# Optimization experiments

Measured on AMD Instinct MI355X. Metric: run time of the kernel, lower is better.

Reference implementation:

```python
import jax, jax.numpy as jnp
import numpy as np

B, CIN, COUT, K, L = 16, 512, 512, 3, 8192
STRIDE, PAD, DIL = 1, 1, 1  # 'same' conv: Lout == L


def setup_inputs() -> dict:
    key = jax.random.key(0)
    k1, k2, k3 = jax.random.split(key, 3)
    x = jax.random.normal(k1, (B, CIN, L), dtype=jnp.float32)
    # int8 quantized weight stored as int32 for portability; values in [-128, 127]
    qweight = jax.random.randint(k2, (COUT, CIN, K), -128, 128, dtype=jnp.int32)
    scale = jnp.float32(0.01)  # per-tensor dequant scale (w_max / 127)
    bias = jax.random.normal(k3, (COUT,), dtype=jnp.float32)
    return {"x": x, "qweight": qweight, "scale": scale, "bias": bias}


def reference(x, qweight, scale, bias):
    # Dequantize: fp32 weight = int8 * scale (materialized every call, as in torch module)
    w = (qweight.astype(jnp.float32) * scale).astype(x.dtype)
    out = jax.lax.conv_general_dilated(
        x, w,
        window_strides=(STRIDE,),
        padding=[(PAD, PAD)],
        rhs_dilation=(DIL,),
        dimension_numbers=("NCH", "OIH", "NCH"),
        feature_group_count=1,
    )
    return out + bias.astype(x.dtype)[None, :, None]
```

## Files before the change

kernel.cpp:

```cpp
#include <hip/hip_runtime.h>
#include <hip/hip_bf16.h>

#define CIN   512
#define COUT  512
#define LEN   8192
#define NB    16
#define KW    3
#define PROWS 8200

#define WB_ELEMS (COUT * CIN * KW)
#define WB_BYTES ((size_t)WB_ELEMS * 2)
#define XS_BYTES ((size_t)NB * PROWS * CIN * 2)

#define BM2 256
#define BN2 256
#define BK3 64
#define NT  ((CIN / BK3) * KW)
#define TILE3 (BM2 * BK3 * 2)

typedef __attribute__((ext_vector_type(4))) float f32x4;
typedef __attribute__((ext_vector_type(8))) short bf16x8;

static __device__ __forceinline__ unsigned short f2bf(float f) {
    union { float f; unsigned u; } cv; cv.f = f;
    return (unsigned short)((cv.u + 0x7fffu + ((cv.u >> 16) & 1u)) >> 16);
}

__global__ __launch_bounds__(256) void wconv_kernel(const int* __restrict__ q,
                                                    unsigned short* __restrict__ wb) {
    int idx = blockIdx.x * 256 + threadIdx.x;
    if (idx >= WB_ELEMS) return;
    int co = idx / (KW * CIN);
    int r  = idx - co * (KW * CIN);
    int t  = r >> 9;
    int ci = r & 511;
    wb[idx] = f2bf((float)q[(co * CIN + ci) * KW + t]);
}

__global__ __launch_bounds__(256) void xprep_kernel(const float* __restrict__ x,
                                                    unsigned short* __restrict__ xs) {
    __shared__ char T[64 * 132];
    int blk = blockIdx.x;
    int b   = blk >> 10;
    int ci0 = ((blk >> 7) & 7) * 64;
    int l0  = (blk & 127) * 64;
    int tid = threadIdx.x;

    if (l0 == 0 && tid < 64)
        xs[((size_t)b * PROWS + 0) * CIN + ci0 + tid] = 0;
    if (l0 == (LEN - 64) && tid < 64)
        xs[((size_t)b * PROWS + (LEN + 1)) * CIN + ci0 + tid] = 0;

    const float* src = x + ((size_t)b * CIN + ci0) * LEN + l0;
    for (int i = tid; i < 64 * 16; i += 256) {
        int r = i >> 4, c4 = i & 15;
        f32x4 v = *(const f32x4*)(src + (size_t)r * LEN + c4 * 4);
        unsigned lo = (unsigned)f2bf(v[0]) | ((unsigned)f2bf(v[1]) << 16);
        unsigned hi = (unsigned)f2bf(v[2]) | ((unsigned)f2bf(v[3]) << 16);
        char* p = T + r * 132 + c4 * 8;
        *(unsigned*)p       = lo;
        *(unsigned*)(p + 4) = hi;
    }
    __syncthreads();
    unsigned short* dst = xs + ((size_t)b * PROWS + 1 + l0) * CIN + ci0;
    for (int i = tid; i < 64 * 8; i += 256) {
        int l = i >> 3, c8 = i & 7;
        union { bf16x8 v; unsigned short s[8]; } pk;
        #pragma unroll
        for (int j = 0; j < 8; ++j)
            pk.s[j] = *(const unsigned short*)(T + (c8 * 8 + j) * 132 + l * 2);
        *(bf16x8*)(dst + (size_t)l * CIN + c8 * 8) = pk.v;
    }
}

__global__ __launch_bounds__(512, 2) void conv_kernel(
    const unsigned short* __restrict__ xs,
    const unsigned short* __restrict__ wb,
    const float* __restrict__ scale_p,
    const float* __restrict__ bias,
    float* __restrict__ out)
{
    __shared__ char sA[2][TILE3];
    __shared__ char sB[2][TILE3];

    const int bid = blockIdx.x;
    const int logical = (bid & 7) * 128 + (bid >> 3);
    const int co_tile = logical & 1;
    const int l_tile  = logical >> 1;
    const int b   = l_tile >> 5;
    const int l0  = (l_tile & 31) * BN2;
    const int co0 = co_tile * BM2;

    const int tid  = threadIdx.x;
    const int lane = tid & 63;
    const int wid  = tid >> 6;
    const int wr   = wid >> 2;
    const int wc   = wid & 3;
    const int lhi  = lane >> 4;
    const int llo  = lane & 15;

    f32x4 acc[8][4] = {};

    const char* xsB = (const char*)(xs + ((size_t)b * PROWS + l0) * CIN);
    const char* wbB = (const char*)wb + (size_t)co0 * (KW * CIN * 2);

    const int it0 = tid, it1 = tid + 512;
    const int r0 = it0 >> 3, r1 = it1 >> 3;
    const int sw0 = ((it0 & 7) * 16) ^ ((r0 & 7) << 4);
    const int sw1 = ((it1 & 7) * 16) ^ ((r1 & 7) << 4);
    const char* pBs[4] = { xsB + r0 * 1024 + sw0,          xsB + r1 * 1024 + sw1,
                           xsB + (128 + r0) * 1024 + sw0,  xsB + (128 + r1) * 1024 + sw1 };
    const char* pAs[4] = { wbB + (size_t)r0 * 3072 + sw0,         wbB + (size_t)r1 * 3072 + sw1,
                           wbB + (size_t)(128 + r0) * 3072 + sw0, wbB + (size_t)(128 + r1) * 3072 + sw1 };
    const int d0 = tid * 16, d1 = d0 + 8192;

    const int s10 = llo & 3, s2 = (llo >> 2) & 1;
    const int constA = (wr * 16 + llo) * 128 + ((lhi ^ s10) << 4);
    const int constB = (wc * 64 + llo) * 128 + ((lhi ^ s10) << 4);
    const char* pA0b = &sA[0][0] + constA + (s2 ? 64 : 0);
    const char* pA1b = &sA[0][0] + constA + (s2 ? 0 : 64);
    const char* pB0b = &sB[0][0] + constB + (s2 ? 64 : 0);
    const char* pB1b = &sB[0][0] + constB + (s2 ? 0 : 64);

#define STAGEU(buf_, u_) do {                                                                \
    const char* s0_; const char* s1_; char* dd_;                                             \
    if ((u_) == 0)      { s0_ = pBs[0]; s1_ = pBs[1]; dd_ = &sB[buf_][0];     }              \
    else if ((u_) == 1) { s0_ = pBs[2]; s1_ = pBs[3]; dd_ = &sB[buf_][16384]; }              \
    else if ((u_) == 2) { s0_ = pAs[0]; s1_ = pAs[1]; dd_ = &sA[buf_][0];     }              \
    else                { s0_ = pAs[2]; s1_ = pAs[3]; dd_ = &sA[buf_][16384]; }              \
    __builtin_amdgcn_global_load_lds(                                                        \
        (const __attribute__((address_space(1))) unsigned int*)s0_,                          \
        (__attribute__((address_space(3))) unsigned int*)(dd_ + d0), 16, 0, 0);              \
    __builtin_amdgcn_global_load_lds(                                                        \
        (const __attribute__((address_space(1))) unsigned int*)s1_,                          \
        (__attribute__((address_space(3))) unsigned int*)(dd_ + d1), 16, 0, 0);              \
    } while (0)

#define RDA(p_, mq_) (*(const bf16x8*)((p_) + (mq_) * 4096))
#define RDB(p_, n_)  (*(const bf16x8*)((p_) + (n_) * 2048))

#define MFMA16(mb_, B0_, B1_, B2_, B3_) do {                                                 \
    __builtin_amdgcn_s_setprio(1);                                                           \
    acc[(mb_)+0][0] = __builtin_amdgcn_mfma_f32_16x16x32_bf16(a0_, B0_, acc[(mb_)+0][0],0,0,0); \
    acc[(mb_)+0][1] = __builtin_amdgcn_mfma_f32_16x16x32_bf16(a0_, B1_, acc[(mb_)+0][1],0,0,0); \
    acc[(mb_)+0][2] = __builtin_amdgcn_mfma_f32_16x16x32_bf16(a0_, B2_, acc[(mb_)+0][2],0,0,0); \
    acc[(mb_)+0][3] = __builtin_amdgcn_mfma_f32_16x16x32_bf16(a0_, B3_, acc[(mb_)+0][3],0,0,0); \
    acc[(mb_)+1][0] = __builtin_amdgcn_mfma_f32_16x16x32_bf16(a1_, B0_, acc[(mb_)+1][0],0,0,0); \
    acc[(mb_)+1][1] = __builtin_amdgcn_mfma_f32_16x16x32_bf16(a1_, B1_, acc[(mb_)+1][1],0,0,0); \
    acc[(mb_)+1][2] = __builtin_amdgcn_mfma_f32_16x16x32_bf16(a1_, B2_, acc[(mb_)+1][2],0,0,0); \
    acc[(mb_)+1][3] = __builtin_amdgcn_mfma_f32_16x16x32_bf16(a1_, B3_, acc[(mb_)+1][3],0,0,0); \
    acc[(mb_)+2][0] = __builtin_amdgcn_mfma_f32_16x16x32_bf16(a2_, B0_, acc[(mb_)+2][0],0,0,0); \
    acc[(mb_)+2][1] = __builtin_amdgcn_mfma_f32_16x16x32_bf16(a2_, B1_, acc[(mb_)+2][1],0,0,0); \
    acc[(mb_)+2][2] = __builtin_amdgcn_mfma_f32_16x16x32_bf16(a2_, B2_, acc[(mb_)+2][2],0,0,0); \
    acc[(mb_)+2][3] = __builtin_amdgcn_mfma_f32_16x16x32_bf16(a2_, B3_, acc[(mb_)+2][3],0,0,0); \
    acc[(mb_)+3][0] = __builtin_amdgcn_mfma_f32_16x16x32_bf16(a3_, B0_, acc[(mb_)+3][0],0,0,0); \
    acc[(mb_)+3][1] = __builtin_amdgcn_mfma_f32_16x16x32_bf16(a3_, B1_, acc[(mb_)+3][1],0,0,0); \
    acc[(mb_)+3][2] = __builtin_amdgcn_mfma_f32_16x16x32_bf16(a3_, B2_, acc[(mb_)+3][2],0,0,0); \
    acc[(mb_)+3][3] = __builtin_amdgcn_mfma_f32_16x16x32_bf16(a3_, B3_, acc[(mb_)+3][3],0,0,0); \
    __builtin_amdgcn_s_setprio(0);                                                           \
    } while (0)

#define BAR()    __builtin_amdgcn_s_barrier()
#define SCHED0() __builtin_amdgcn_sched_barrier(0)
#define LGKM0()  asm volatile("s_waitcnt lgkmcnt(0)" ::: "memory")

    STAGEU(0, 0); STAGEU(0, 1); STAGEU(0, 2); STAGEU(0, 3);
    {
        #pragma unroll
        for (int i = 0; i < 4; ++i) { pBs[i] += 1024; pAs[i] += 1024; }
    }
    int tapn = 1;
    asm volatile("s_waitcnt vmcnt(2)" ::: "memory");
    BAR();

    bf16x8 a0_, a1_, a2_, a3_;
    bf16x8 bk00, bk01, bk02, bk03;
    bf16x8 bk10, bk11, bk12, bk13;

    #pragma unroll 1
    for (int c = 0; c < NT - 1; ++c) {
        const int buf = c & 1, nb = buf ^ 1;
        const int bufo = buf << 15;
        const char* cpA0 = pA0b + bufo;
        const char* cpA1 = pA1b + bufo;
        const char* cpB0 = pB0b + bufo;
        const char* cpB1 = pB1b + bufo;

        SCHED0();
        bk00 = RDB(cpB0, 0); bk01 = RDB(cpB0, 1); bk02 = RDB(cpB0, 2); bk03 = RDB(cpB0, 3);
        a0_ = RDA(cpA0, 0); a1_ = RDA(cpA0, 1); a2_ = RDA(cpA0, 2); a3_ = RDA(cpA0, 3);
        STAGEU(nb, 0);
        BAR(); LGKM0(); SCHED0();
        MFMA16(0, bk00, bk01, bk02, bk03);
        BAR();
        SCHED0();
        bk10 = RDB(cpB1, 0); bk11 = RDB(cpB1, 1); bk12 = RDB(cpB1, 2); bk13 = RDB(cpB1, 3);
        a0_ = RDA(cpA1, 0); a1_ = RDA(cpA1, 1); a2_ = RDA(cpA1, 2); a3_ = RDA(cpA1, 3);
        STAGEU(nb, 1);
        asm volatile("s_waitcnt vmcnt(4)" ::: "memory");
        BAR(); LGKM0(); SCHED0();
        MFMA16(0, bk10, bk11, bk12, bk13);
        BAR();
        SCHED0();
        a0_ = RDA(cpA0, 4); a1_ = RDA(cpA0, 5); a2_ = RDA(cpA0, 6); a3_ = RDA(cpA0, 7);
        STAGEU(nb, 2);
        BAR(); LGKM0(); SCHED0();
        MFMA16(4, bk00, bk01, bk02, bk03);
        BAR();
        SCHED0();
        a0_ = RDA(cpA1, 4); a1_ = RDA(cpA1, 5); a2_ = RDA(cpA1, 6); a3_ = RDA(cpA1, 7);
        STAGEU(nb, 3);
        asm volatile("s_waitcnt vmcnt(2)" ::: "memory");
        BAR(); LGKM0(); SCHED0();
        MFMA16(4, bk10, bk11, bk12, bk13);
        BAR();

        const int kd = (tapn == 2) ? -1920 : 1024;
        tapn = (tapn == 2) ? 0 : tapn + 1;
        #pragma unroll
        for (int i = 0; i < 4; ++i) { pBs[i] += kd; pAs[i] += kd; }
    }
    {
        const int bufo = ((NT - 1) & 1) << 15;
        const char* cpA0 = pA0b + bufo;
        const char* cpA1 = pA1b + bufo;
        const char* cpB0 = pB0b + bufo;
        const char* cpB1 = pB1b + bufo;
        SCHED0();
        bk00 = RDB(cpB0, 0); bk01 = RDB(cpB0, 1); bk02 = RDB(cpB0, 2); bk03 = RDB(cpB0, 3);
        a0_ = RDA(cpA0, 0); a1_ = RDA(cpA0, 1); a2_ = RDA(cpA0, 2); a3_ = RDA(cpA0, 3);
        BAR(); LGKM0(); SCHED0();
        MFMA16(0, bk00, bk01, bk02, bk03);
        BAR();
        SCHED0();
        bk10 = RDB(cpB1, 0); bk11 = RDB(cpB1, 1); bk12 = RDB(cpB1, 2); bk13 = RDB(cpB1, 3);
        a0_ = RDA(cpA1, 0); a1_ = RDA(cpA1, 1); a2_ = RDA(cpA1, 2); a3_ = RDA(cpA1, 3);
        asm volatile("s_waitcnt vmcnt(0)" ::: "memory");
        BAR(); LGKM0(); SCHED0();
        MFMA16(0, bk10, bk11, bk12, bk13);
        BAR();
        SCHED0();
        a0_ = RDA(cpA0, 4); a1_ = RDA(cpA0, 5); a2_ = RDA(cpA0, 6); a3_ = RDA(cpA0, 7);
        BAR(); LGKM0(); SCHED0();
        MFMA16(4, bk00, bk01, bk02, bk03);
        BAR();
        SCHED0();
        a0_ = RDA(cpA1, 4); a1_ = RDA(cpA1, 5); a2_ = RDA(cpA1, 6); a3_ = RDA(cpA1, 7);
        LGKM0(); SCHED0();
        MFMA16(4, bk10, bk11, bk12, bk13);
    }
#undef STAGEU
#undef RDA
#undef RDB
#undef MFMA16

    const float sc = scale_p[0];
    #pragma unroll
    for (int m = 0; m < 8; ++m) {
        #pragma unroll
        for (int j = 0; j < 4; ++j) {
            int co = co0 + m * 32 + wr * 16 + lhi * 4 + j;
            float bv = bias[co];
            size_t orow = ((size_t)b * COUT + co) * LEN + l0 + wc * 64;
            #pragma unroll
            for (int n = 0; n < 4; ++n)
                out[orow + n * 16 + llo] = sc * acc[m][n][j] + bv;
        }
    }
}

__global__ __launch_bounds__(256, 2) void conv_fb_kernel(
    const float* __restrict__ x,
    const unsigned short* __restrict__ wb,
    const float* __restrict__ scale_p,
    const float* __restrict__ bias,
    float* __restrict__ out)
{
    __shared__ char xT[132 * 128];
    const int bid = blockIdx.x;
    const int logical = (bid & 7) * 512 + (bid >> 3);
    const int co_tile = logical & 3;
    const int n_tile  = logical >> 2;
    const int b   = n_tile >> 6;
    const int l0  = (n_tile & 63) * 128;
    const int co0 = co_tile * 128;
    const int tid  = threadIdx.x;
    const int lane = tid & 63;
    const int wid  = tid >> 6;
    const int wr = wid >> 1, wc = wid & 1;
    const int lhi = lane >> 4;
    const int llo = lane & 15;
    f32x4 acc[4][4] = {};
    const float* xb = x + (size_t)b * CIN * LEN;

    for (int ci0 = 0; ci0 < CIN; ci0 += 64) {
        __syncthreads();
        for (int it = tid; it < 132 * 8; it += 256) {
            int c = it % 132;
            int o = it / 132;
            int l = l0 - 1 + c;
            float v[8];
            if (l >= 0 && l < LEN) {
                const float* src = xb + (size_t)(ci0 + o * 8) * LEN + l;
                #pragma unroll
                for (int j = 0; j < 8; ++j) v[j] = src[(size_t)j * LEN];
            } else {
                #pragma unroll
                for (int j = 0; j < 8; ++j) v[j] = 0.f;
            }
            union { bf16x8 v8; unsigned short s[8]; } pk;
            #pragma unroll
            for (int j = 0; j < 8; ++j) pk.s[j] = f2bf(v[j]);
            int byte = c * 128 + ((o * 16) ^ ((c & 7) << 4));
            *reinterpret_cast<bf16x8*>(xT + byte) = pk.v8;
        }
        __syncthreads();
        #pragma unroll
        for (int t = 0; t < KW; ++t) {
            #pragma unroll
            for (int s = 0; s < 2; ++s) {
                bf16x8 af[4];
                #pragma unroll
                for (int m = 0; m < 4; ++m)
                    af[m] = *reinterpret_cast<const bf16x8*>(
                        wb + (size_t)(co0 + wr * 64 + m * 16 + llo) * (KW * CIN)
                           + t * CIN + ci0 + s * 32 + 8 * lhi);
                bf16x8 bfr[4];
                #pragma unroll
                for (int n = 0; n < 4; ++n) {
                    int col = wc * 64 + n * 16 + llo + t;
                    int byte = col * 128 + (((s * 32 + 8 * lhi) * 2) ^ ((col & 7) << 4));
                    bfr[n] = *reinterpret_cast<const bf16x8*>(xT + byte);
                }
                #pragma unroll
                for (int m = 0; m < 4; ++m)
                    #pragma unroll
                    for (int n = 0; n < 4; ++n)
                        acc[m][n] = __builtin_amdgcn_mfma_f32_16x16x32_bf16(af[m], bfr[n], acc[m][n], 0, 0, 0);
            }
        }
    }
    const float sc = scale_p[0];
    #pragma unroll
    for (int m = 0; m < 4; ++m) {
        #pragma unroll
        for (int j = 0; j < 4; ++j) {
            int co = co0 + wr * 64 + m * 16 + lhi * 4 + j;
            float bv = bias[co];
            size_t orow = ((size_t)b * COUT + co) * LEN + l0 + wc * 64;
            #pragma unroll
            for (int n = 0; n < 4; ++n)
                out[orow + n * 16 + llo] = sc * acc[m][n][j] + bv;
        }
    }
}

extern "C" void kernel_launch(void* const* d_in, const int* in_sizes, int n_in,
                              void* d_out, int out_size, void* d_ws, size_t ws_size,
                              hipStream_t stream) {
    const float* x    = (const float*)d_in[0];
    const int*   qw   = (const int*)d_in[1];
    const float* sc   = (const float*)d_in[2];
    const float* bias = (const float*)d_in[3];
    float* out = (float*)d_out;
    unsigned short* wb = (unsigned short*)d_ws;

    wconv_kernel<<<(WB_ELEMS + 255) / 256, 256, 0, stream>>>(qw, wb);

    if (ws_size >= WB_BYTES + XS_BYTES) {
        unsigned short* xsw = (unsigned short*)((char*)d_ws + WB_BYTES);
        xprep_kernel<<<NB * 8 * (LEN / 64), 256, 0, stream>>>(x, xsw);
        conv_kernel<<<(COUT / BM2) * (NB * LEN / BN2), 512, 0, stream>>>(xsw, wb, sc, bias, out);
    } else {
        conv_fb_kernel<<<4096, 256, 0, stream>>>(x, wb, sc, bias, out);
    }
}
```

Before: 301.1 us.

## Double-buffer MFMA operand registers to overlap LDS reads with MFMA

Adds a second set of A/B fragment registers so each quarter-step's LDS reads are issued before the previous fragment's MFMA block, and the first fragment of the next K-tile is prefetched at the end of the iteration. The explicit lgkmcnt(0) waits are removed, so LDS latency hides behind MFMA work instead of stalling before each block. This costs extra VGPRs and relies on the compiler inserting correct waits. Barrier placement shifts, so prefetching from the next buffer depends on the vmcnt waits staying correct.

```diff
diff --git a/kernel.cpp b/kernel.cpp
--- a/kernel.cpp
+++ b/kernel.cpp
@@ -139,30 +139,29 @@
 #define RDA(p_, mq_) (*(const bf16x8*)((p_) + (mq_) * 4096))
 #define RDB(p_, n_)  (*(const bf16x8*)((p_) + (n_) * 2048))
 
-#define MFMA16(mb_, B0_, B1_, B2_, B3_) do {                                                 \
+#define MFMA16(mb_, A0_, A1_, A2_, A3_, B0_, B1_, B2_, B3_) do {                             \
     __builtin_amdgcn_s_setprio(1);                                                           \
-    acc[(mb_)+0][0] = __builtin_amdgcn_mfma_f32_16x16x32_bf16(a0_, B0_, acc[(mb_)+0][0],0,0,0); \
-    acc[(mb_)+0][1] = __builtin_amdgcn_mfma_f32_16x16x32_bf16(a0_, B1_, acc[(mb_)+0][1],0,0,0); \
-    acc[(mb_)+0][2] = __builtin_amdgcn_mfma_f32_16x16x32_bf16(a0_, B2_, acc[(mb_)+0][2],0,0,0); \
-    acc[(mb_)+0][3] = __builtin_amdgcn_mfma_f32_16x16x32_bf16(a0_, B3_, acc[(mb_)+0][3],0,0,0); \
-    acc[(mb_)+1][0] = __builtin_amdgcn_mfma_f32_16x16x32_bf16(a1_, B0_, acc[(mb_)+1][0],0,0,0); \
-    acc[(mb_)+1][1] = __builtin_amdgcn_mfma_f32_16x16x32_bf16(a1_, B1_, acc[(mb_)+1][1],0,0,0); \
-    acc[(mb_)+1][2] = __builtin_amdgcn_mfma_f32_16x16x32_bf16(a1_, B2_, acc[(mb_)+1][2],0,0,0); \
-    acc[(mb_)+1][3] = __builtin_amdgcn_mfma_f32_16x16x32_bf16(a1_, B3_, acc[(mb_)+1][3],0,0,0); \
-    acc[(mb_)+2][0] = __builtin_amdgcn_mfma_f32_16x16x32_bf16(a2_, B0_, acc[(mb_)+2][0],0,0,0); \
-    acc[(mb_)+2][1] = __builtin_amdgcn_mfma_f32_16x16x32_bf16(a2_, B1_, acc[(mb_)+2][1],0,0,0); \
-    acc[(mb_)+2][2] = __builtin_amdgcn_mfma_f32_16x16x32_bf16(a2_, B2_, acc[(mb_)+2][2],0,0,0); \
-    acc[(mb_)+2][3] = __builtin_amdgcn_mfma_f32_16x16x32_bf16(a2_, B3_, acc[(mb_)+2][3],0,0,0); \
-    acc[(mb_)+3][0] = __builtin_amdgcn_mfma_f32_16x16x32_bf16(a3_, B0_, acc[(mb_)+3][0],0,0,0); \
-    acc[(mb_)+3][1] = __builtin_amdgcn_mfma_f32_16x16x32_bf16(a3_, B1_, acc[(mb_)+3][1],0,0,0); \
-    acc[(mb_)+3][2] = __builtin_amdgcn_mfma_f32_16x16x32_bf16(a3_, B2_, acc[(mb_)+3][2],0,0,0); \
-    acc[(mb_)+3][3] = __builtin_amdgcn_mfma_f32_16x16x32_bf16(a3_, B3_, acc[(mb_)+3][3],0,0,0); \
+    acc[(mb_)+0][0] = __builtin_amdgcn_mfma_f32_16x16x32_bf16(A0_, B0_, acc[(mb_)+0][0],0,0,0); \
+    acc[(mb_)+0][1] = __builtin_amdgcn_mfma_f32_16x16x32_bf16(A0_, B1_, acc[(mb_)+0][1],0,0,0); \
+    acc[(mb_)+0][2] = __builtin_amdgcn_mfma_f32_16x16x32_bf16(A0_, B2_, acc[(mb_)+0][2],0,0,0); \
+    acc[(mb_)+0][3] = __builtin_amdgcn_mfma_f32_16x16x32_bf16(A0_, B3_, acc[(mb_)+0][3],0,0,0); \
+    acc[(mb_)+1][0] = __builtin_amdgcn_mfma_f32_16x16x32_bf16(A1_, B0_, acc[(mb_)+1][0],0,0,0); \
+    acc[(mb_)+1][1] = __builtin_amdgcn_mfma_f32_16x16x32_bf16(A1_, B1_, acc[(mb_)+1][1],0,0,0); \
+    acc[(mb_)+1][2] = __builtin_amdgcn_mfma_f32_16x16x32_bf16(A1_, B2_, acc[(mb_)+1][2],0,0,0); \
+    acc[(mb_)+1][3] = __builtin_amdgcn_mfma_f32_16x16x32_bf16(A1_, B3_, acc[(mb_)+1][3],0,0,0); \
+    acc[(mb_)+2][0] = __builtin_amdgcn_mfma_f32_16x16x32_bf16(A2_, B0_, acc[(mb_)+2][0],0,0,0); \
+    acc[(mb_)+2][1] = __builtin_amdgcn_mfma_f32_16x16x32_bf16(A2_, B1_, acc[(mb_)+2][1],0,0,0); \
+    acc[(mb_)+2][2] = __builtin_amdgcn_mfma_f32_16x16x32_bf16(A2_, B2_, acc[(mb_)+2][2],0,0,0); \
+    acc[(mb_)+2][3] = __builtin_amdgcn_mfma_f32_16x16x32_bf16(A2_, B3_, acc[(mb_)+2][3],0,0,0); \
+    acc[(mb_)+3][0] = __builtin_amdgcn_mfma_f32_16x16x32_bf16(A3_, B0_, acc[(mb_)+3][0],0,0,0); \
+    acc[(mb_)+3][1] = __builtin_amdgcn_mfma_f32_16x16x32_bf16(A3_, B1_, acc[(mb_)+3][1],0,0,0); \
+    acc[(mb_)+3][2] = __builtin_amdgcn_mfma_f32_16x16x32_bf16(A3_, B2_, acc[(mb_)+3][2],0,0,0); \
+    acc[(mb_)+3][3] = __builtin_amdgcn_mfma_f32_16x16x32_bf16(A3_, B3_, acc[(mb_)+3][3],0,0,0); \
     __builtin_amdgcn_s_setprio(0);                                                           \
     } while (0)
 
 #define BAR()    __builtin_amdgcn_s_barrier()
 #define SCHED0() __builtin_amdgcn_sched_barrier(0)
-#define LGKM0()  asm volatile("s_waitcnt lgkmcnt(0)" ::: "memory")
 
     STAGEU(0, 0); STAGEU(0, 1); STAGEU(0, 2); STAGEU(0, 3);
     {
@@ -171,48 +170,62 @@
     }
     int tapn = 1;
     asm volatile("s_waitcnt vmcnt(2)" ::: "memory");
-    BAR();
-
-    bf16x8 a0_, a1_, a2_, a3_;
-    bf16x8 bk00, bk01, bk02, bk03;
-    bf16x8 bk10, bk11, bk12, bk13;
+    BAR(); SCHED0();
+
+    bf16x8 aX0, aX1, aX2, aX3;
+    bf16x8 aY0, aY1, aY2, aY3;
+    bf16x8 bA0, bA1, bA2, bA3;
+    bf16x8 bB0, bB1, bB2, bB3;
+
+    aX0 = RDA(pA0b, 0); aX1 = RDA(pA0b, 1); aX2 = RDA(pA0b, 2); aX3 = RDA(pA0b, 3);
+    bA0 = RDB(pB0b, 0); bA1 = RDB(pB0b, 1); bA2 = RDB(pB0b, 2); bA3 = RDB(pB0b, 3);
 
     #pragma unroll 1
     for (int c = 0; c < NT - 1; ++c) {
-        const int buf = c & 1, nb = buf ^ 1;
-        const int bufo = buf << 15;
+        const int buf = c & 1;
+        const int nb  = buf ^ 1;
+        const int bufo = buf << 15, nbo = nb << 15;
         const char* cpA0 = pA0b + bufo;
         const char* cpA1 = pA1b + bufo;
-        const char* cpB0 = pB0b + bufo;
         const char* cpB1 = pB1b + bufo;
-
-        SCHED0();
-        bk00 = RDB(cpB0, 0); bk01 = RDB(cpB0, 1); bk02 = RDB(cpB0, 2); bk03 = RDB(cpB0, 3);
-        a0_ = RDA(cpA0, 0); a1_ = RDA(cpA0, 1); a2_ = RDA(cpA0, 2); a3_ = RDA(cpA0, 3);
+        const char* npA0 = pA0b + nbo;
+        const char* npB0 = pB0b + nbo;
+
+        SCHED0();
         STAGEU(nb, 0);
-        BAR(); LGKM0(); SCHED0();
-        MFMA16(0, bk00, bk01, bk02, bk03);
-        BAR();
-        SCHED0();
-        bk10 = RDB(cpB1, 0); bk11 = RDB(cpB1, 1); bk12 = RDB(cpB1, 2); bk13 = RDB(cpB1, 3);
-        a0_ = RDA(cpA1, 0); a1_ = RDA(cpA1, 1); a2_ = RDA(cpA1, 2); a3_ = RDA(cpA1, 3);
+        SCHED0();
+        BAR(); SCHED0();
+        aY0 = RDA(cpA1, 0); aY1 = RDA(cpA1, 1); aY2 = RDA(cpA1, 2); aY3 = RDA(cpA1, 3);
+        bB0 = RDB(cpB1, 0); bB1 = RDB(cpB1, 1); bB2 = RDB(cpB1, 2); bB3 = RDB(cpB1, 3);
+        SCHED0();
+        MFMA16(0, aX0, aX1, aX2, aX3, bA0, bA1, bA2, bA3);
+        BAR();
+        SCHED0();
         STAGEU(nb, 1);
         asm volatile("s_waitcnt vmcnt(4)" ::: "memory");
-        BAR(); LGKM0(); SCHED0();
-        MFMA16(0, bk10, bk11, bk12, bk13);
-        BAR();
-        SCHED0();
-        a0_ = RDA(cpA0, 4); a1_ = RDA(cpA0, 5); a2_ = RDA(cpA0, 6); a3_ = RDA(cpA0, 7);
+        SCHED0();
+        BAR(); SCHED0();
+        aX0 = RDA(cpA0, 4); aX1 = RDA(cpA0, 5); aX2 = RDA(cpA0, 6); aX3 = RDA(cpA0, 7);
+        SCHED0();
+        MFMA16(0, aY0, aY1, aY2, aY3, bB0, bB1, bB2, bB3);
+        BAR();
+        SCHED0();
         STAGEU(nb, 2);
-        BAR(); LGKM0(); SCHED0();
-        MFMA16(4, bk00, bk01, bk02, bk03);
-        BAR();
-        SCHED0();
-        a0_ = RDA(cpA1, 4); a1_ = RDA(cpA1, 5); a2_ = RDA(cpA1, 6); a3_ = RDA(cpA1, 7);
+        SCHED0();
+        BAR(); SCHED0();
+        aY0 = RDA(cpA1, 4); aY1 = RDA(cpA1, 5); aY2 = RDA(cpA1, 6); aY3 = RDA(cpA1, 7);
+        SCHED0();
+        MFMA16(4, aX0, aX1, aX2, aX3, bA0, bA1, bA2, bA3);
+        BAR();
+        SCHED0();
         STAGEU(nb, 3);
         asm volatile("s_waitcnt vmcnt(2)" ::: "memory");
-        BAR(); LGKM0(); SCHED0();
-        MFMA16(4, bk10, bk11, bk12, bk13);
+        SCHED0();
+        BAR(); SCHED0();
+        aX0 = RDA(npA0, 0); aX1 = RDA(npA0, 1); aX2 = RDA(npA0, 2); aX3 = RDA(npA0, 3);
+        bA0 = RDB(npB0, 0); bA1 = RDB(npB0, 1); bA2 = RDB(npB0, 2); bA3 = RDB(npB0, 3);
+        SCHED0();
+        MFMA16(4, aY0, aY1, aY2, aY3, bB0, bB1, bB2, bB3);
         BAR();
 
         const int kd = (tapn == 2) ? -1920 : 1024;
@@ -224,30 +237,25 @@
         const int bufo = ((NT - 1) & 1) << 15;
         const char* cpA0 = pA0b + bufo;
         const char* cpA1 = pA1b + bufo;
-        const char* cpB0 = pB0b + bufo;
         const char* cpB1 = pB1b + bufo;
         SCHED0();
-        bk00 = RDB(cpB0, 0); bk01 = RDB(cpB0, 1); bk02 = RDB(cpB0, 2); bk03 = RDB(cpB0, 3);
-        a0_ = RDA(cpA0, 0); a1_ = RDA(cpA0, 1); a2_ = RDA(cpA0, 2); a3_ = RDA(cpA0, 3);
-        BAR(); LGKM0(); SCHED0();
-        MFMA16(0, bk00, bk01, bk02, bk03);
-        BAR();
-        SCHED0();
-        bk10 = RDB(cpB1, 0); bk11 = RDB(cpB1, 1); bk12 = RDB(cpB1, 2); bk13 = RDB(cpB1, 3);
-        a0_ = RDA(cpA1, 0); a1_ = RDA(cpA1, 1); a2_ = RDA(cpA1, 2); a3_ = RDA(cpA1, 3);
+        aY0 = RDA(cpA1, 0); aY1 = RDA(cpA1, 1); aY2 = RDA(cpA1, 2); aY3 = RDA(cpA1, 3);
+        bB0 = RDB(cpB1, 0); bB1 = RDB(cpB1, 1); bB2 = RDB(cpB1, 2); bB3 = RDB(cpB1, 3);
+        SCHED0();
+        MFMA16(0, aX0, aX1, aX2, aX3, bA0, bA1, bA2, bA3);
+        BAR();
         asm volatile("s_waitcnt vmcnt(0)" ::: "memory");
-        BAR(); LGKM0(); SCHED0();
-        MFMA16(0, bk10, bk11, bk12, bk13);
-        BAR();
-        SCHED0();
-        a0_ = RDA(cpA0, 4); a1_ = RDA(cpA0, 5); a2_ = RDA(cpA0, 6); a3_ = RDA(cpA0, 7);
-        BAR(); LGKM0(); SCHED0();
-        MFMA16(4, bk00, bk01, bk02, bk03);
-        BAR();
-        SCHED0();
-        a0_ = RDA(cpA1, 4); a1_ = RDA(cpA1, 5); a2_ = RDA(cpA1, 6); a3_ = RDA(cpA1, 7);
-        LGKM0(); SCHED0();
-        MFMA16(4, bk10, bk11, bk12, bk13);
+        BAR(); SCHED0();
+        aX0 = RDA(cpA0, 4); aX1 = RDA(cpA0, 5); aX2 = RDA(cpA0, 6); aX3 = RDA(cpA0, 7);
+        SCHED0();
+        MFMA16(0, aY0, aY1, aY2, aY3, bB0, bB1, bB2, bB3);
+        BAR();
+        SCHED0();
+        aY0 = RDA(cpA1, 4); aY1 = RDA(cpA1, 5); aY2 = RDA(cpA1, 6); aY3 = RDA(cpA1, 7);
+        SCHED0();
+        MFMA16(4, aX0, aX1, aX2, aX3, bA0, bA1, bA2, bA3);
+        SCHED0();
+        MFMA16(4, aY0, aY1, aY2, aY3, bB0, bB1, bB2, bB3);
     }
 #undef STAGEU
 #undef RDA
```

Result: slower. 456.1 us (+51.5%).
